# Kernel tuning notes

Measured on AMD Instinct MI355X. Metric: run time of the kernel, lower is better.

The kernel has to match this reference:

```python
import jax, jax.numpy as jnp
import numpy as np

B, S, D = 1, 4096, 768
H = 12
HD = D // H  # head_dim = 64


def setup_inputs() -> dict:
    key = jax.random.key(0)
    ks = jax.random.split(key, 5)
    std = 1.0 / np.sqrt(D)
    return {
        "x": jax.random.normal(ks[0], (B, S, D), dtype=jnp.float32),
        "w_k": jax.random.normal(ks[1], (D, D), dtype=jnp.float32) * std,
        "w_q": jax.random.normal(ks[2], (D, D), dtype=jnp.float32) * std,
        "w_v": jax.random.normal(ks[3], (D, D), dtype=jnp.float32) * std,
        "w_o": jax.random.normal(ks[4], (D, D), dtype=jnp.float32) * std,
        "b_o": jnp.zeros((D,), dtype=jnp.float32),
    }


def reference(x, w_k, w_q, w_v, w_o, b_o):
    b, n, _ = x.shape
    # Projections (Linear without bias): y = x @ W^T; weights stored [out, in]
    q = (x @ w_q.T).reshape(b, n, H, HD)
    k = (x @ w_k.T).reshape(b, n, H, HD)
    v = (x @ w_v.T).reshape(b, n, H, HD)
    # [b, h, s_q, s_k] attention scores (naive full matrix, as in source)
    scores = jnp.einsum("bqhd,bkhd->bhqk", q, k)
    causal = jnp.tril(jnp.ones((n, n), dtype=bool))  # True = keep
    scores = jnp.where(causal[None, None], scores, -jnp.inf)
    attn = jax.nn.softmax(scores / np.sqrt(HD).astype(np.float32), axis=-1)
    # dropout p=0.0 -> identity (eval mode)
    ctx = jnp.einsum("bhqk,bkhd->bqhd", attn, v).reshape(b, n, D)
    return ctx @ w_o.T + b_o
```

## Files before the change

### kernel.cpp

```cpp
#include <hip/hip_runtime.h>
#include <math.h>

#define S_LEN   4096
#define D_MODEL 768
#define N_HEAD  12
#define H_DIM   64
#define NELEM   (S_LEN * D_MODEL)
#define WELEM   (D_MODEL * D_MODEL)

typedef unsigned short ushort;
typedef __attribute__((ext_vector_type(8))) short short8;
typedef __attribute__((ext_vector_type(4))) float f32x4;

__device__ __forceinline__ ushort f2bh(float f) {
  unsigned u = __float_as_uint(f);
  u += 0x7fffu + ((u >> 16) & 1u);
  return (ushort)(u >> 16);
}
__device__ __forceinline__ float bh2f(ushort h) {
  return __uint_as_float(((unsigned)h) << 16);
}

#define SWZ(row, colByte) ((((row) * 128) + (colByte)) ^ (((row) & 7) << 4))

__global__ __launch_bounds__(256)
void convert_x(const float* __restrict__ x, ushort* __restrict__ xh,
               ushort* __restrict__ xl) {
  size_t i = ((size_t)blockIdx.x * 256 + threadIdx.x) * 4;
  float4 v = *reinterpret_cast<const float4*>(&x[i]);
  ushort4 hv, lv;
  hv.x = f2bh(v.x); lv.x = f2bh(v.x - bh2f(hv.x));
  hv.y = f2bh(v.y); lv.y = f2bh(v.y - bh2f(hv.y));
  hv.z = f2bh(v.z); lv.z = f2bh(v.z - bh2f(hv.z));
  hv.w = f2bh(v.w); lv.w = f2bh(v.w - bh2f(hv.w));
  *reinterpret_cast<ushort4*>(&xh[i]) = hv;
  *reinterpret_cast<ushort4*>(&xl[i]) = lv;
}

__global__ __launch_bounds__(256)
void convert_w(const float* __restrict__ wq, const float* __restrict__ wk,
               const float* __restrict__ wv, const float* __restrict__ wo,
               ushort* __restrict__ WH, ushort* __restrict__ WL) {
  int z = blockIdx.z;
  const float* src = (z == 0) ? wq : (z == 1) ? wk : (z == 2) ? wv : wo;
  ushort* oh = WH + (size_t)z * WELEM;
  ushort* ol = WL + (size_t)z * WELEM;
  size_t i = ((size_t)blockIdx.x * 256 + threadIdx.x) * 4;
  float4 v = *reinterpret_cast<const float4*>(&src[i]);
  ushort4 hv, lv;
  hv.x = f2bh(v.x); lv.x = f2bh(v.x - bh2f(hv.x));
  hv.y = f2bh(v.y); lv.y = f2bh(v.y - bh2f(hv.y));
  hv.z = f2bh(v.z); lv.z = f2bh(v.z - bh2f(hv.z));
  hv.w = f2bh(v.w); lv.w = f2bh(v.w - bh2f(hv.w));
  *reinterpret_cast<ushort4*>(&oh[i]) = hv;
  *reinterpret_cast<ushort4*>(&ol[i]) = lv;
}

__device__ __forceinline__ void gemm_bf3_core(
    const ushort* __restrict__ Ah, const ushort* __restrict__ Al,
    const ushort* __restrict__ Wh, const ushort* __restrict__ Wl,
    int rowbase, int colbase, f32x4 (&acc)[4][2]) {
  __shared__ __align__(16) ushort AhS[128 * 64];
  __shared__ __align__(16) ushort AlS[128 * 64];
  __shared__ __align__(16) ushort WhS[64 * 64];
  __shared__ __align__(16) ushort WlS[64 * 64];
  char* AhB = (char*)AhS; char* AlB = (char*)AlS;
  char* WhB = (char*)WhS; char* WlB = (char*)WlS;

  const int tid  = threadIdx.x;
  const int lane = tid & 63;
  const int w    = tid >> 6;
  const int wm   = w >> 1;
  const int wn   = w & 1;
  const int lr   = lane & 15;
  const int lk   = lane >> 4;

  const int r0 = tid >> 3;
  const int cb = (tid & 7) * 16;
  const int ce = (tid & 7) * 8;
  const int sA0 = SWZ(r0, cb);
  const int sA1 = SWZ(r0 + 32, cb);
  const int sA2 = SWZ(r0 + 64, cb);
  const int sA3 = SWZ(r0 + 96, cb);

#pragma unroll
  for (int mt = 0; mt < 4; ++mt)
#pragma unroll
    for (int nt = 0; nt < 2; ++nt) acc[mt][nt] = {0.f, 0.f, 0.f, 0.f};

  float4 gA0h, gA1h, gA2h, gA3h, gA0l, gA1l, gA2l, gA3l;
  float4 gW0h, gW1h, gW0l, gW1l;

#define GEMM_ISSUE(k0_)                                                     \
  {                                                                         \
    size_t oA = (size_t)(rowbase + r0) * D_MODEL + (k0_) + ce;              \
    const size_t st = 32 * (size_t)D_MODEL;                                 \
    gA0h = *reinterpret_cast<const float4*>(Ah + oA);                       \
    gA1h = *reinterpret_cast<const float4*>(Ah + oA + st);                  \
    gA2h = *reinterpret_cast<const float4*>(Ah + oA + 2 * st);              \
    gA3h = *reinterpret_cast<const float4*>(Ah + oA + 3 * st);              \
    gA0l = *reinterpret_cast<const float4*>(Al + oA);                       \
    gA1l = *reinterpret_cast<const float4*>(Al + oA + st);                  \
    gA2l = *reinterpret_cast<const float4*>(Al + oA + 2 * st);              \
    gA3l = *reinterpret_cast<const float4*>(Al + oA + 3 * st);              \
    size_t oW = (size_t)(colbase + r0) * D_MODEL + (k0_) + ce;              \
    gW0h = *reinterpret_cast<const float4*>(Wh + oW);                       \
    gW1h = *reinterpret_cast<const float4*>(Wh + oW + st);                  \
    gW0l = *reinterpret_cast<const float4*>(Wl + oW);                       \
    gW1l = *reinterpret_cast<const float4*>(Wl + oW + st);                  \
  }

  GEMM_ISSUE(0);
  for (int ks = 0; ks < D_MODEL / 64; ++ks) {
    __syncthreads();
    *reinterpret_cast<float4*>(AhB + sA0) = gA0h;
    *reinterpret_cast<float4*>(AhB + sA1) = gA1h;
    *reinterpret_cast<float4*>(AhB + sA2) = gA2h;
    *reinterpret_cast<float4*>(AhB + sA3) = gA3h;
    *reinterpret_cast<float4*>(AlB + sA0) = gA0l;
    *reinterpret_cast<float4*>(AlB + sA1) = gA1l;
    *reinterpret_cast<float4*>(AlB + sA2) = gA2l;
    *reinterpret_cast<float4*>(AlB + sA3) = gA3l;
    *reinterpret_cast<float4*>(WhB + sA0) = gW0h;
    *reinterpret_cast<float4*>(WhB + sA1) = gW1h;
    *reinterpret_cast<float4*>(WlB + sA0) = gW0l;
    *reinterpret_cast<float4*>(WlB + sA1) = gW1l;
    __syncthreads();
    if (ks < D_MODEL / 64 - 1) GEMM_ISSUE((ks + 1) * 64);

#pragma unroll
    for (int kc = 0; kc < 2; ++kc) {
      short8 ah[4], al[4], bh[2], bl[2];
#pragma unroll
      for (int mt = 0; mt < 4; ++mt) {
        int o = SWZ(wm * 64 + mt * 16 + lr, kc * 64 + lk * 16);
        ah[mt] = *reinterpret_cast<const short8*>(AhB + o);
        al[mt] = *reinterpret_cast<const short8*>(AlB + o);
      }
#pragma unroll
      for (int nt = 0; nt < 2; ++nt) {
        int o = SWZ(wn * 32 + nt * 16 + lr, kc * 64 + lk * 16);
        bh[nt] = *reinterpret_cast<const short8*>(WhB + o);
        bl[nt] = *reinterpret_cast<const short8*>(WlB + o);
      }
#pragma unroll
      for (int mt = 0; mt < 4; ++mt)
#pragma unroll
        for (int nt = 0; nt < 2; ++nt) {
          acc[mt][nt] = __builtin_amdgcn_mfma_f32_16x16x32_bf16(
              ah[mt], bh[nt], acc[mt][nt], 0, 0, 0);
          acc[mt][nt] = __builtin_amdgcn_mfma_f32_16x16x32_bf16(
              al[mt], bh[nt], acc[mt][nt], 0, 0, 0);
          acc[mt][nt] = __builtin_amdgcn_mfma_f32_16x16x32_bf16(
              ah[mt], bl[nt], acc[mt][nt], 0, 0, 0);
        }
    }
  }
#undef GEMM_ISSUE
}

__global__ __launch_bounds__(256)
void gemm_qkv_bf3(const ushort* __restrict__ xh, const ushort* __restrict__ xl,
                  const ushort* __restrict__ WH, const ushort* __restrict__ WL,
                  ushort* __restrict__ QKV) {
  const int z = blockIdx.z;
  const ushort* Wh = WH + (size_t)z * WELEM;
  const ushort* Wl = WL + (size_t)z * WELEM;
  ushort* oh = QKV + (size_t)z * (2 * NELEM);
  ushort* ol = oh + NELEM;
  const float scale = (z == 0) ? 0.125f * 1.44269504089f : 1.0f;
  const int rowbase = blockIdx.y * 128;
  const int colbase = blockIdx.x * 64;

  f32x4 acc[4][2];
  gemm_bf3_core(xh, xl, Wh, Wl, rowbase, colbase, acc);

  const int lane = threadIdx.x & 63, w = threadIdx.x >> 6;
  const int wm = w >> 1, wn = w & 1, lr = lane & 15, lk = lane >> 4;
#pragma unroll
  for (int mt = 0; mt < 4; ++mt)
#pragma unroll
    for (int nt = 0; nt < 2; ++nt)
#pragma unroll
      for (int j = 0; j < 4; ++j) {
        int rg = rowbase + wm * 64 + mt * 16 + lk * 4 + j;
        int cg = colbase + wn * 32 + nt * 16 + lr;
        float v = acc[mt][nt][j] * scale;
        ushort hh = f2bh(v);
        oh[(size_t)rg * D_MODEL + cg] = hh;
        ol[(size_t)rg * D_MODEL + cg] = f2bh(v - bh2f(hh));
      }
}

__global__ __launch_bounds__(256)
void gemm_out_bf3(const ushort* __restrict__ ch, const ushort* __restrict__ cl,
                  const ushort* __restrict__ woh, const ushort* __restrict__ wol,
                  const float* __restrict__ bo, float* __restrict__ out) {
  const int rowbase = blockIdx.y * 128;
  const int colbase = blockIdx.x * 64;
  f32x4 acc[4][2];
  gemm_bf3_core(ch, cl, woh, wol, rowbase, colbase, acc);

  const int lane = threadIdx.x & 63, w = threadIdx.x >> 6;
  const int wm = w >> 1, wn = w & 1, lr = lane & 15, lk = lane >> 4;
#pragma unroll
  for (int nt = 0; nt < 2; ++nt) {
    int cg = colbase + wn * 32 + nt * 16 + lr;
    float bb = bo[cg];
#pragma unroll
    for (int mt = 0; mt < 4; ++mt)
#pragma unroll
      for (int j = 0; j < 4; ++j) {
        int rg = rowbase + wm * 64 + mt * 16 + lk * 4 + j;
        out[(size_t)rg * D_MODEL + cg] = acc[mt][nt][j] + bb;
      }
  }
}

__global__ __launch_bounds__(256)
void convert_vt(const ushort* __restrict__ Vrh, const ushort* __restrict__ Vrl,
                ushort* __restrict__ Vth, ushort* __restrict__ Vtl) {
  __shared__ ushort th[64][68];
  __shared__ ushort tl[64][68];
  const int tid = threadIdx.x;
  const int s0  = blockIdx.x * 64;
  const int h   = blockIdx.y;
#pragma unroll
  for (int it = 0; it < 4; ++it) {
    int id = tid + it * 256;
    int s  = id >> 4;
    int c4 = (id & 15) * 4;
    size_t g = (size_t)(s0 + s) * D_MODEL + h * H_DIM + c4;
    ushort4 vh = *reinterpret_cast<const ushort4*>(&Vrh[g]);
    ushort4 vl = *reinterpret_cast<const ushort4*>(&Vrl[g]);
    th[c4 + 0][s] = vh.x; th[c4 + 1][s] = vh.y;
    th[c4 + 2][s] = vh.z; th[c4 + 3][s] = vh.w;
    tl[c4 + 0][s] = vl.x; tl[c4 + 1][s] = vl.y;
    tl[c4 + 2][s] = vl.z; tl[c4 + 3][s] = vl.w;
  }
  __syncthreads();
#pragma unroll
  for (int it = 0; it < 4; ++it) {
    int id = tid + it * 256;
    int d  = id >> 4;
    int s4 = (id & 15) * 4;
    ushort4 oh, ol;
    oh.x = th[d][s4 + 0]; oh.y = th[d][s4 + 1];
    oh.z = th[d][s4 + 2]; oh.w = th[d][s4 + 3];
    ol.x = tl[d][s4 + 0]; ol.y = tl[d][s4 + 1];
    ol.z = tl[d][s4 + 2]; ol.w = tl[d][s4 + 3];
    size_t o = (size_t)(h * H_DIM + d) * S_LEN + s0 + s4;
    *reinterpret_cast<ushort4*>(&Vth[o]) = oh;
    *reinterpret_cast<ushort4*>(&Vtl[o]) = ol;
  }
}

__global__ __launch_bounds__(256)
void attn_mfma(const ushort* __restrict__ Qh_g, const ushort* __restrict__ Ql_g,
               const ushort* __restrict__ Kh_g, const ushort* __restrict__ Kl_g,
               const ushort* __restrict__ Vh_g, const ushort* __restrict__ Vl_g,
               ushort* __restrict__ CTXh, ushort* __restrict__ CTXl,
               float* __restrict__ O_part, float* __restrict__ m_part,
               float* __restrict__ l_part) {
  const int bxl = blockIdx.x;
  const int h   = bxl % N_HEAD;
  const int i   = bxl / N_HEAD;
  int qb, c = 0, nch = 1, slot = 0, partial = 0;
  if (i < 8) {
    qb = 15 - i;
  } else if (i < 152) {
    int j = i - 8;
    if (j < 64)       { qb = 63 - (j >> 2);        c = j & 3;        nch = 4; }
    else if (j < 112) { int off = j - 64;  qb = 47 - off / 3; c = off % 3; nch = 3; }
    else              { int off = j - 112; qb = 31 - off / 2; c = off & 1; nch = 2; }
    partial = 1;
    slot = h * 144 + j;
  } else {
    qb = 159 - i;
  }
  const int kt0 = c * (qb + 1) / nch;
  const int kt1 = (c + 1) * (qb + 1) / nch;

  __shared__ __align__(16) ushort Kh_s[64 * 64];
  __shared__ __align__(16) ushort Kl_s[64 * 64];
  __shared__ __align__(16) ushort Vh_s[64 * 64];
  __shared__ __align__(16) ushort Vl_s[64 * 64];
  __shared__ __align__(16) ushort P_s[4][16 * 64];

  char* KhB = (char*)Kh_s;
  char* KlB = (char*)Kl_s;
  char* VhB = (char*)Vh_s;
  char* VlB = (char*)Vl_s;

  const int tid  = threadIdx.x;
  const int lane = tid & 63;
  const int w    = tid >> 6;
  const int lr   = lane & 15;
  const int lk   = lane >> 4;
  const float NEG = -1e30f;

  const int r0 = tid >> 3;
  const int cb = (tid & 7) * 16;
  const int ce = (tid & 7) * 8;
  const int swA = SWZ(r0, cb);
  const int swB = SWZ(r0 + 32, cb);

  {
    size_t g0 = (size_t)(qb * 64 + r0) * D_MODEL + h * H_DIM + ce;
    size_t g1 = g0 + 32 * (size_t)D_MODEL;
    *reinterpret_cast<float4*>(KhB + swA) =
        *reinterpret_cast<const float4*>(Qh_g + g0);
    *reinterpret_cast<float4*>(KhB + swB) =
        *reinterpret_cast<const float4*>(Qh_g + g1);
    *reinterpret_cast<float4*>(KlB + swA) =
        *reinterpret_cast<const float4*>(Ql_g + g0);
    *reinterpret_cast<float4*>(KlB + swB) =
        *reinterpret_cast<const float4*>(Ql_g + g1);
  }
  __syncthreads();
  short8 aqh[2], aql[2];
#pragma unroll
  for (int kc = 0; kc < 2; ++kc) {
    int ao = SWZ(w * 16 + lr, kc * 64 + lk * 16);
    aqh[kc] = *reinterpret_cast<const short8*>(KhB + ao);
    aql[kc] = *reinterpret_cast<const short8*>(KlB + ao);
  }

  f32x4 o[4];
  float m[4], l[4];
#pragma unroll
  for (int t = 0; t < 4; ++t) o[t] = {0.f, 0.f, 0.f, 0.f};
#pragma unroll
  for (int r = 0; r < 4; ++r) { m[r] = NEG; l[r] = 0.f; }

  float4 gkh0, gkh1, gkl0, gkl1, gvh0, gvh1, gvl0, gvl1;

#define ATTN_ISSUE(kt_)                                                     \
  {                                                                         \
    size_t gk0 = (size_t)((kt_) * 64 + r0) * D_MODEL + h * H_DIM + ce;      \
    size_t gk1 = gk0 + 32 * (size_t)D_MODEL;                                \
    size_t gv0 = (size_t)(h * H_DIM + r0) * S_LEN + (kt_) * 64 + ce;        \
    size_t gv1 = gv0 + 32 * (size_t)S_LEN;                                  \
    gkh0 = *reinterpret_cast<const float4*>(Kh_g + gk0);                    \
    gkh1 = *reinterpret_cast<const float4*>(Kh_g + gk1);                    \
    gkl0 = *reinterpret_cast<const float4*>(Kl_g + gk0);                    \
    gkl1 = *reinterpret_cast<const float4*>(Kl_g + gk1);                    \
    gvh0 = *reinterpret_cast<const float4*>(Vh_g + gv0);                    \
    gvh1 = *reinterpret_cast<const float4*>(Vh_g + gv1);                    \
    gvl0 = *reinterpret_cast<const float4*>(Vl_g + gv0);                    \
    gvl1 = *reinterpret_cast<const float4*>(Vl_g + gv1);                    \
  }

  ATTN_ISSUE(kt0);

  for (int kt = kt0; kt < kt1; ++kt) {
    __syncthreads();
    *reinterpret_cast<float4*>(KhB + swA) = gkh0;
    *reinterpret_cast<float4*>(KhB + swB) = gkh1;
    *reinterpret_cast<float4*>(KlB + swA) = gkl0;
    *reinterpret_cast<float4*>(KlB + swB) = gkl1;
    *reinterpret_cast<float4*>(VhB + swA) = gvh0;
    *reinterpret_cast<float4*>(VhB + swB) = gvh1;
    *reinterpret_cast<float4*>(VlB + swA) = gvl0;
    *reinterpret_cast<float4*>(VlB + swB) = gvl1;
    __syncthreads();
    if (kt + 1 < kt1) ATTN_ISSUE(kt + 1);

    f32x4 sacc[4];
#pragma unroll
    for (int t = 0; t < 4; ++t) sacc[t] = {0.f, 0.f, 0.f, 0.f};
#pragma unroll
    for (int kc = 0; kc < 2; ++kc) {
#pragma unroll
      for (int t = 0; t < 4; ++t) {
        int bo = SWZ(t * 16 + lr, kc * 64 + lk * 16);
        short8 bh = *reinterpret_cast<const short8*>(KhB + bo);
        short8 bl = *reinterpret_cast<const short8*>(KlB + bo);
        sacc[t] = __builtin_amdgcn_mfma_f32_16x16x32_bf16(aqh[kc], bh, sacc[t], 0, 0, 0);
        sacc[t] = __builtin_amdgcn_mfma_f32_16x16x32_bf16(aql[kc], bh, sacc[t], 0, 0, 0);
        sacc[t] = __builtin_amdgcn_mfma_f32_16x16x32_bf16(aqh[kc], bl, sacc[t], 0, 0, 0);
      }
    }

    if (kt == qb) {
#pragma unroll
      for (int t = 0; t < 4; ++t) {
        int colg = t * 16 + lr;
#pragma unroll
        for (int r = 0; r < 4; ++r) {
          int rowg = w * 16 + lk * 4 + r;
          if (colg > rowg) sacc[t][r] = NEG;
        }
      }
    }

    float pf[4][4];
#pragma unroll
    for (int r = 0; r < 4; ++r) {
      float mx = fmaxf(fmaxf(sacc[0][r], sacc[1][r]),
                       fmaxf(sacc[2][r], sacc[3][r]));
      mx = fmaxf(mx, __shfl_xor(mx, 1));
      mx = fmaxf(mx, __shfl_xor(mx, 2));
      mx = fmaxf(mx, __shfl_xor(mx, 4));
      mx = fmaxf(mx, __shfl_xor(mx, 8));
      if (__any(mx > m[r])) {
        float mnew  = fmaxf(m[r], mx);
        float alpha = exp2f(m[r] - mnew);
        m[r] = mnew;
        l[r] *= alpha;
#pragma unroll
        for (int t = 0; t < 4; ++t) o[t][r] *= alpha;
      }
      float p0 = exp2f(sacc[0][r] - m[r]);
      float p1 = exp2f(sacc[1][r] - m[r]);
      float p2 = exp2f(sacc[2][r] - m[r]);
      float p3 = exp2f(sacc[3][r] - m[r]);
      pf[0][r] = p0; pf[1][r] = p1; pf[2][r] = p2; pf[3][r] = p3;
      l[r] += (p0 + p1) + (p2 + p3);
    }

    char* pwB = (char*)P_s[w];
#pragma unroll
    for (int r = 0; r < 4; ++r) {
      int prow = lk * 4 + r;
#pragma unroll
      for (int t = 0; t < 4; ++t) {
        int off = SWZ(prow, (t * 16 + lr) * 2);
        *reinterpret_cast<ushort*>(pwB + off) = f2bh(pf[t][r]);
      }
    }

#pragma unroll
    for (int kc = 0; kc < 2; ++kc) {
      short8 pa = *reinterpret_cast<const short8*>(
          pwB + SWZ(lr, kc * 64 + lk * 16));
#pragma unroll
      for (int t = 0; t < 4; ++t) {
        int bo = SWZ(t * 16 + lr, kc * 64 + lk * 16);
        short8 vh = *reinterpret_cast<const short8*>(VhB + bo);
        short8 vl = *reinterpret_cast<const short8*>(VlB + bo);
        o[t] = __builtin_amdgcn_mfma_f32_16x16x32_bf16(pa, vh, o[t], 0, 0, 0);
        o[t] = __builtin_amdgcn_mfma_f32_16x16x32_bf16(pa, vl, o[t], 0, 0, 0);
      }
    }
  }
#undef ATTN_ISSUE

#pragma unroll
  for (int r = 0; r < 4; ++r) {
    l[r] += __shfl_xor(l[r], 1);
    l[r] += __shfl_xor(l[r], 2);
    l[r] += __shfl_xor(l[r], 4);
    l[r] += __shfl_xor(l[r], 8);
  }

  if (!partial) {
    float inv[4];
#pragma unroll
    for (int r = 0; r < 4; ++r) inv[r] = 1.f / l[r];
#pragma unroll
    for (int t = 0; t < 4; ++t)
#pragma unroll
      for (int r = 0; r < 4; ++r) {
        size_t idx = (size_t)(qb * 64 + w * 16 + lk * 4 + r) * D_MODEL +
                     h * H_DIM + t * 16 + lr;
        float v = o[t][r] * inv[r];
        ushort hh = f2bh(v);
        CTXh[idx] = hh;
        CTXl[idx] = f2bh(v - bh2f(hh));
      }
  } else {
    float* Ob = O_part + (size_t)slot * 4096;
#pragma unroll
    for (int t = 0; t < 4; ++t)
#pragma unroll
      for (int r = 0; r < 4; ++r)
        Ob[(w * 16 + lk * 4 + r) * 64 + t * 16 + lr] = o[t][r];
    if (lr == 0) {
#pragma unroll
      for (int r = 0; r < 4; ++r) {
        int row = w * 16 + lk * 4 + r;
        m_part[slot * 64 + row] = m[r];
        l_part[slot * 64 + row] = l[r];
      }
    }
  }
}

__global__ __launch_bounds__(256)
void attn_combine(const float* __restrict__ O_part,
                  const float* __restrict__ m_part,
                  const float* __restrict__ l_part,
                  ushort* __restrict__ CTXh, ushort* __restrict__ CTXl) {
  const int qb  = 16 + blockIdx.x;
  const int h   = blockIdx.y;
  const int tid = threadIdx.x;
  const int row = tid >> 2;
  const int d0  = (tid & 3) * 16;
  int nch, sbl;
  if (qb >= 48)      { nch = 4; sbl = (63 - qb) * 4; }
  else if (qb >= 32) { nch = 3; sbl = 64 + (47 - qb) * 3; }
  else               { nch = 2; sbl = 112 + (31 - qb) * 2; }
  const int sb = h * 144 + sbl;
  const int s2 = (nch >= 3) ? sb + 2 : sb;
  const int s3 = (nch >= 4) ? sb + 3 : sb;

  float m0 = m_part[(sb + 0) * 64 + row];
  float m1 = m_part[(sb + 1) * 64 + row];
  float m2 = (nch >= 3) ? m_part[s2 * 64 + row] : -1e30f;
  float m3 = (nch >= 4) ? m_part[s3 * 64 + row] : -1e30f;
  float l0 = l_part[(sb + 0) * 64 + row];
  float l1 = l_part[(sb + 1) * 64 + row];
  float l2 = (nch >= 3) ? l_part[s2 * 64 + row] : 0.f;
  float l3 = (nch >= 4) ? l_part[s3 * 64 + row] : 0.f;
  float M  = fmaxf(fmaxf(m0, m1), fmaxf(m2, m3));
  float a0 = exp2f(m0 - M);
  float a1 = exp2f(m1 - M);
  float a2 = (nch >= 3) ? exp2f(m2 - M) : 0.f;
  float a3 = (nch >= 4) ? exp2f(m3 - M) : 0.f;
  float inv = 1.0f / (l0 * a0 + l1 * a1 + l2 * a2 + l3 * a3);

  const float* p0 = O_part + (size_t)(sb + 0) * 4096 + row * 64 + d0;
  const float* p1 = O_part + (size_t)(sb + 1) * 4096 + row * 64 + d0;
  const float* p2 = O_part + (size_t)s2 * 4096 + row * 64 + d0;
  const float* p3 = O_part + (size_t)s3 * 4096 + row * 64 + d0;
  size_t ob = (size_t)(qb * 64 + row) * D_MODEL + h * H_DIM + d0;
#pragma unroll
  for (int j = 0; j < 16; j += 4) {
    float4 x0 = *reinterpret_cast<const float4*>(p0 + j);
    float4 x1 = *reinterpret_cast<const float4*>(p1 + j);
    float4 x2 = *reinterpret_cast<const float4*>(p2 + j);
    float4 x3 = *reinterpret_cast<const float4*>(p3 + j);
    float4 v;
    v.x = (x0.x * a0 + x1.x * a1 + x2.x * a2 + x3.x * a3) * inv;
    v.y = (x0.y * a0 + x1.y * a1 + x2.y * a2 + x3.y * a3) * inv;
    v.z = (x0.z * a0 + x1.z * a1 + x2.z * a2 + x3.z * a3) * inv;
    v.w = (x0.w * a0 + x1.w * a1 + x2.w * a2 + x3.w * a3) * inv;
    ushort4 hv, lv;
    hv.x = f2bh(v.x); lv.x = f2bh(v.x - bh2f(hv.x));
    hv.y = f2bh(v.y); lv.y = f2bh(v.y - bh2f(hv.y));
    hv.z = f2bh(v.z); lv.z = f2bh(v.z - bh2f(hv.z));
    hv.w = f2bh(v.w); lv.w = f2bh(v.w - bh2f(hv.w));
    *reinterpret_cast<ushort4*>(&CTXh[ob + j]) = hv;
    *reinterpret_cast<ushort4*>(&CTXl[ob + j]) = lv;
  }
}

extern "C" void kernel_launch(void* const* d_in, const int* in_sizes, int n_in,
                              void* d_out, int out_size, void* d_ws,
                              size_t ws_size, hipStream_t stream) {
  const float* x  = (const float*)d_in[0];
  const float* wk = (const float*)d_in[1];
  const float* wq = (const float*)d_in[2];
  const float* wv = (const float*)d_in[3];
  const float* wo = (const float*)d_in[4];
  const float* bo = (const float*)d_in[5];
  float* out = (float*)d_out;

  ushort* xh   = (ushort*)d_ws;
  ushort* xl   = xh + NELEM;
  ushort* WH   = xl + NELEM;
  ushort* WL   = WH + 4 * (size_t)WELEM;
  ushort* QKV  = WL + 4 * (size_t)WELEM;
  ushort* Qh   = QKV;
  ushort* Ql   = Qh + NELEM;
  ushort* Kh   = Ql + NELEM;
  ushort* Kl   = Kh + NELEM;
  ushort* Vrh  = Kl + NELEM;
  ushort* Vrl  = Vrh + NELEM;
  ushort* Vth  = Vrl + NELEM;
  ushort* Vtl  = Vth + NELEM;
  ushort* CTXh = Vrh;
  ushort* CTXl = Vrl;
  float* O_part = (float*)(Vtl + NELEM);
  float* m_part = O_part + 1728 * (size_t)4096;
  float* l_part = m_part + 1728 * 64;

  dim3 blk(256);
  convert_x<<<dim3(NELEM / 4 / 256), blk, 0, stream>>>(x, xh, xl);
  convert_w<<<dim3(WELEM / 4 / 256, 1, 4), blk, 0, stream>>>(wq, wk, wv, wo,
                                                             WH, WL);
  gemm_qkv_bf3<<<dim3(D_MODEL / 64, S_LEN / 128, 3), blk, 0, stream>>>(
      xh, xl, WH, WL, QKV);
  convert_vt<<<dim3(S_LEN / 64, N_HEAD), blk, 0, stream>>>(Vrh, Vrl, Vth, Vtl);
  attn_mfma<<<dim3(160 * N_HEAD), blk, 0, stream>>>(
      Qh, Ql, Kh, Kl, Vth, Vtl, CTXh, CTXl, O_part, m_part, l_part);
  attn_combine<<<dim3(48, N_HEAD), blk, 0, stream>>>(O_part, m_part, l_part,
                                                     CTXh, CTXl);
  gemm_out_bf3<<<dim3(D_MODEL / 64, S_LEN / 128, 1), blk, 0, stream>>>(
      CTXh, CTXl, WH + 3 * (size_t)WELEM, WL + 3 * (size_t)WELEM, bo, out);
}
```

Baseline: 314.6 us.

## Transpose QK^T MFMA so softmax rows live per lane; pass P via shuffles

The S = QK^T MFMA operands are swapped so each lane holds one query row's scores. The row max and sum then need only two cross-lane shuffles instead of four per row, with a single m/l scalar per lane. The probability tile no longer goes through a shared-memory P buffer. It is packed to bf16 with v_cvt_pk_bf16_f32 and redistributed into the PV A-operand layout with register shuffles, which removes LDS writes and reads per tile. Global K/V addresses are now incremented rather than recomputed. The cost is extra shuffles for the alpha and 1/l broadcasts and for building the P operand.

```diff
diff --git a/kernel.cpp b/kernel.cpp
--- a/kernel.cpp
+++ b/kernel.cpp
@@ -11,6 +11,7 @@
 typedef unsigned short ushort;
 typedef __attribute__((ext_vector_type(8))) short short8;
 typedef __attribute__((ext_vector_type(4))) float f32x4;
+typedef __attribute__((ext_vector_type(4))) int i32x4;
 
 __device__ __forceinline__ ushort f2bh(float f) {
   unsigned u = __float_as_uint(f);
@@ -19,6 +20,11 @@
 }
 __device__ __forceinline__ float bh2f(ushort h) {
   return __uint_as_float(((unsigned)h) << 16);
+}
+__device__ __forceinline__ unsigned cvtpk_bf16(float a, float b) {
+  unsigned r;
+  asm("v_cvt_pk_bf16_f32 %0, %1, %2" : "=v"(r) : "v"(a), "v"(b));
+  return r;
 }
 
 #define SWZ(row, colByte) ((((row) * 128) + (colByte)) ^ (((row) & 7) << 4))
@@ -285,7 +291,6 @@
   __shared__ __align__(16) ushort Kl_s[64 * 64];
   __shared__ __align__(16) ushort Vh_s[64 * 64];
   __shared__ __align__(16) ushort Vl_s[64 * 64];
-  __shared__ __align__(16) ushort P_s[4][16 * 64];
 
   char* KhB = (char*)Kh_s;
   char* KlB = (char*)Kl_s;
@@ -327,20 +332,18 @@
   }
 
   f32x4 o[4];
-  float m[4], l[4];
+  float m = NEG, l = 0.f;
 #pragma unroll
   for (int t = 0; t < 4; ++t) o[t] = {0.f, 0.f, 0.f, 0.f};
-#pragma unroll
-  for (int r = 0; r < 4; ++r) { m[r] = NEG; l[r] = 0.f; }
 
   float4 gkh0, gkh1, gkl0, gkl1, gvh0, gvh1, gvl0, gvl1;
-
-#define ATTN_ISSUE(kt_)                                                     \
+  size_t gk0 = (size_t)(kt0 * 64 + r0) * D_MODEL + h * H_DIM + ce;
+  size_t gk1 = gk0 + 32 * (size_t)D_MODEL;
+  size_t gv0 = (size_t)(h * H_DIM + r0) * S_LEN + kt0 * 64 + ce;
+  size_t gv1 = gv0 + 32 * (size_t)S_LEN;
+
+#define ATTN_ISSUE()                                                        \
   {                                                                         \
-    size_t gk0 = (size_t)((kt_) * 64 + r0) * D_MODEL + h * H_DIM + ce;      \
-    size_t gk1 = gk0 + 32 * (size_t)D_MODEL;                                \
-    size_t gv0 = (size_t)(h * H_DIM + r0) * S_LEN + (kt_) * 64 + ce;        \
-    size_t gv1 = gv0 + 32 * (size_t)S_LEN;                                  \
     gkh0 = *reinterpret_cast<const float4*>(Kh_g + gk0);                    \
     gkh1 = *reinterpret_cast<const float4*>(Kh_g + gk1);                    \
     gkl0 = *reinterpret_cast<const float4*>(Kl_g + gk0);                    \
@@ -349,9 +352,11 @@
     gvh1 = *reinterpret_cast<const float4*>(Vh_g + gv1);                    \
     gvl0 = *reinterpret_cast<const float4*>(Vl_g + gv0);                    \
     gvl1 = *reinterpret_cast<const float4*>(Vl_g + gv1);                    \
-  }
-
-  ATTN_ISSUE(kt0);
+    gk0 += 64 * (size_t)D_MODEL; gk1 += 64 * (size_t)D_MODEL;               \
+    gv0 += 64; gv1 += 64;                                                   \
+  }
+
+  ATTN_ISSUE();
 
   for (int kt = kt0; kt < kt1; ++kt) {
     __syncthreads();
@@ -364,7 +369,7 @@
     *reinterpret_cast<float4*>(VlB + swA) = gvl0;
     *reinterpret_cast<float4*>(VlB + swB) = gvl1;
     __syncthreads();
-    if (kt + 1 < kt1) ATTN_ISSUE(kt + 1);
+    if (kt + 1 < kt1) ATTN_ISSUE();
 
     f32x4 sacc[4];
 #pragma unroll
@@ -374,101 +379,106 @@
 #pragma unroll
       for (int t = 0; t < 4; ++t) {
         int bo = SWZ(t * 16 + lr, kc * 64 + lk * 16);
-        short8 bh = *reinterpret_cast<const short8*>(KhB + bo);
-        short8 bl = *reinterpret_cast<const short8*>(KlB + bo);
-        sacc[t] = __builtin_amdgcn_mfma_f32_16x16x32_bf16(aqh[kc], bh, sacc[t], 0, 0, 0);
-        sacc[t] = __builtin_amdgcn_mfma_f32_16x16x32_bf16(aql[kc], bh, sacc[t], 0, 0, 0);
-        sacc[t] = __builtin_amdgcn_mfma_f32_16x16x32_bf16(aqh[kc], bl, sacc[t], 0, 0, 0);
+        short8 kh = *reinterpret_cast<const short8*>(KhB + bo);
+        short8 kl = *reinterpret_cast<const short8*>(KlB + bo);
+        sacc[t] = __builtin_amdgcn_mfma_f32_16x16x32_bf16(kh, aqh[kc], sacc[t], 0, 0, 0);
+        sacc[t] = __builtin_amdgcn_mfma_f32_16x16x32_bf16(kl, aqh[kc], sacc[t], 0, 0, 0);
+        sacc[t] = __builtin_amdgcn_mfma_f32_16x16x32_bf16(kh, aql[kc], sacc[t], 0, 0, 0);
       }
     }
 
     if (kt == qb) {
+      int qloc = w * 16 + lr;
+#pragma unroll
+      for (int t = 0; t < 4; ++t)
+#pragma unroll
+        for (int r = 0; r < 4; ++r)
+          if (t * 16 + lk * 4 + r > qloc) sacc[t][r] = NEG;
+    }
+
+    float mx = fmaxf(fmaxf(fmaxf(sacc[0][0], sacc[0][1]),
+                           fmaxf(sacc[0][2], sacc[0][3])),
+                     fmaxf(fmaxf(sacc[1][0], sacc[1][1]),
+                           fmaxf(sacc[1][2], sacc[1][3])));
+    mx = fmaxf(mx, fmaxf(fmaxf(fmaxf(sacc[2][0], sacc[2][1]),
+                               fmaxf(sacc[2][2], sacc[2][3])),
+                         fmaxf(fmaxf(sacc[3][0], sacc[3][1]),
+                               fmaxf(sacc[3][2], sacc[3][3]))));
+    mx = fmaxf(mx, __shfl_xor(mx, 16));
+    mx = fmaxf(mx, __shfl_xor(mx, 32));
+    if (__any(mx > m)) {
+      float mnew  = fmaxf(m, mx);
+      float alpha = exp2f(m - mnew);
+      m = mnew;
+      l *= alpha;
+      int bsrc = (lane & 48) | (((lane >> 4) & 3) << 2);
+#pragma unroll
+      for (int r = 0; r < 4; ++r) {
+        float ar = __shfl(alpha, bsrc + r);
+#pragma unroll
+        for (int t = 0; t < 4; ++t) o[t][r] *= ar;
+      }
+    }
+    unsigned u0[4], u1[4];
+#pragma unroll
+    for (int t = 0; t < 4; ++t) {
+      float p0 = exp2f(sacc[t][0] - m);
+      float p1 = exp2f(sacc[t][1] - m);
+      float p2 = exp2f(sacc[t][2] - m);
+      float p3 = exp2f(sacc[t][3] - m);
+      l += (p0 + p1) + (p2 + p3);
+      u0[t] = cvtpk_bf16(p0, p1);
+      u1[t] = cvtpk_bf16(p2, p3);
+    }
+
+    {
+      int srcA = ((2 * (lk & 1)) << 4) | lr;
+      int srcB = srcA + 16;
+      int hi   = (lk >> 1) & 1;
+#pragma unroll
+      for (int kc = 0; kc < 2; ++kc) {
+        unsigned aA0 = __shfl(u0[2 * kc], srcA), bA0 = __shfl(u0[2 * kc + 1], srcA);
+        unsigned aA1 = __shfl(u1[2 * kc], srcA), bA1 = __shfl(u1[2 * kc + 1], srcA);
+        unsigned aB0 = __shfl(u0[2 * kc], srcB), bB0 = __shfl(u0[2 * kc + 1], srcB);
+        unsigned aB1 = __shfl(u1[2 * kc], srcB), bB1 = __shfl(u1[2 * kc + 1], srcB);
+        i32x4 tv;
+        tv[0] = (int)(hi ? bA0 : aA0);
+        tv[1] = (int)(hi ? bA1 : aA1);
+        tv[2] = (int)(hi ? bB0 : aB0);
+        tv[3] = (int)(hi ? bB1 : aB1);
+        short8 pa = __builtin_bit_cast(short8, tv);
+#pragma unroll
+        for (int t = 0; t < 4; ++t) {
+          int bo = SWZ(t * 16 + lr, kc * 64 + lk * 16);
+          short8 vh = *reinterpret_cast<const short8*>(VhB + bo);
+          short8 vl = *reinterpret_cast<const short8*>(VlB + bo);
+          o[t] = __builtin_amdgcn_mfma_f32_16x16x32_bf16(pa, vh, o[t], 0, 0, 0);
+          o[t] = __builtin_amdgcn_mfma_f32_16x16x32_bf16(pa, vl, o[t], 0, 0, 0);
+        }
+      }
+    }
+  }
+#undef ATTN_ISSUE
+
+  l += __shfl_xor(l, 16);
+  l += __shfl_xor(l, 32);
+
+  if (!partial) {
+    float rl = 1.f / l;
+    int bsrc = (lane & 48) | (((lane >> 4) & 3) << 2);
+#pragma unroll
+    for (int r = 0; r < 4; ++r) {
+      float invr = __shfl(rl, bsrc + r);
 #pragma unroll
       for (int t = 0; t < 4; ++t) {
-        int colg = t * 16 + lr;
-#pragma unroll
-        for (int r = 0; r < 4; ++r) {
-          int rowg = w * 16 + lk * 4 + r;
-          if (colg > rowg) sacc[t][r] = NEG;
-        }
-      }
-    }
-
-    float pf[4][4];
-#pragma unroll
-    for (int r = 0; r < 4; ++r) {
-      float mx = fmaxf(fmaxf(sacc[0][r], sacc[1][r]),
-                       fmaxf(sacc[2][r], sacc[3][r]));
-      mx = fmaxf(mx, __shfl_xor(mx, 1));
-      mx = fmaxf(mx, __shfl_xor(mx, 2));
-      mx = fmaxf(mx, __shfl_xor(mx, 4));
-      mx = fmaxf(mx, __shfl_xor(mx, 8));
-      if (__any(mx > m[r])) {
-        float mnew  = fmaxf(m[r], mx);
-        float alpha = exp2f(m[r] - mnew);
-        m[r] = mnew;
-        l[r] *= alpha;
-#pragma unroll
-        for (int t = 0; t < 4; ++t) o[t][r] *= alpha;
-      }
-      float p0 = exp2f(sacc[0][r] - m[r]);
-      float p1 = exp2f(sacc[1][r] - m[r]);
-      float p2 = exp2f(sacc[2][r] - m[r]);
-      float p3 = exp2f(sacc[3][r] - m[r]);
-      pf[0][r] = p0; pf[1][r] = p1; pf[2][r] = p2; pf[3][r] = p3;
-      l[r] += (p0 + p1) + (p2 + p3);
-    }
-
-    char* pwB = (char*)P_s[w];
-#pragma unroll
-    for (int r = 0; r < 4; ++r) {
-      int prow = lk * 4 + r;
-#pragma unroll
-      for (int t = 0; t < 4; ++t) {
-        int off = SWZ(prow, (t * 16 + lr) * 2);
-        *reinterpret_cast<ushort*>(pwB + off) = f2bh(pf[t][r]);
-      }
-    }
-
-#pragma unroll
-    for (int kc = 0; kc < 2; ++kc) {
-      short8 pa = *reinterpret_cast<const short8*>(
-          pwB + SWZ(lr, kc * 64 + lk * 16));
-#pragma unroll
-      for (int t = 0; t < 4; ++t) {
-        int bo = SWZ(t * 16 + lr, kc * 64 + lk * 16);
-        short8 vh = *reinterpret_cast<const short8*>(VhB + bo);
-        short8 vl = *reinterpret_cast<const short8*>(VlB + bo);
-        o[t] = __builtin_amdgcn_mfma_f32_16x16x32_bf16(pa, vh, o[t], 0, 0, 0);
-        o[t] = __builtin_amdgcn_mfma_f32_16x16x32_bf16(pa, vl, o[t], 0, 0, 0);
-      }
-    }
-  }
-#undef ATTN_ISSUE
-
-#pragma unroll
-  for (int r = 0; r < 4; ++r) {
-    l[r] += __shfl_xor(l[r], 1);
-    l[r] += __shfl_xor(l[r], 2);
-    l[r] += __shfl_xor(l[r], 4);
-    l[r] += __shfl_xor(l[r], 8);
-  }
-
-  if (!partial) {
-    float inv[4];
-#pragma unroll
-    for (int r = 0; r < 4; ++r) inv[r] = 1.f / l[r];
-#pragma unroll
-    for (int t = 0; t < 4; ++t)
-#pragma unroll
-      for (int r = 0; r < 4; ++r) {
         size_t idx = (size_t)(qb * 64 + w * 16 + lk * 4 + r) * D_MODEL +
                      h * H_DIM + t * 16 + lr;
-        float v = o[t][r] * inv[r];
+        float v = o[t][r] * invr;
         ushort hh = f2bh(v);
         CTXh[idx] = hh;
         CTXl[idx] = f2bh(v - bh2f(hh));
       }
+    }
   } else {
     float* Ob = O_part + (size_t)slot * 4096;
 #pragma unroll
@@ -476,13 +486,9 @@
 #pragma unroll
       for (int r = 0; r < 4; ++r)
         Ob[(w * 16 + lk * 4 + r) * 64 + t * 16 + lr] = o[t][r];
-    if (lr == 0) {
-#pragma unroll
-      for (int r = 0; r < 4; ++r) {
-        int row = w * 16 + lk * 4 + r;
-        m_part[slot * 64 + row] = m[r];
-        l_part[slot * 64 + row] = l[r];
-      }
+    if ((lane >> 4) == 0) {
+      m_part[slot * 64 + w * 16 + lr] = m;
+      l_part[slot * 64 + w * 16 + lr] = l;
     }
   }
 }
```

Result: faster. 278.5 us (-11.5%).
